# Performance work log

Measured on AMD Instinct MI355X. Metric: run time of the kernel, lower is better.

Reference implementation:

```python
import jax, jax.numpy as jnp
import numpy as np

B, T, C, H = 2, 2048, 1024, 16
HD = C // H  # head dim = 64


def setup_inputs() -> dict:
    key = jax.random.key(0)
    ks = jax.random.split(key, 5)
    scale = 0.02
    return {
        "x": jax.random.normal(ks[0], (B, T, C), dtype=jnp.float32),
        "W_attn": jax.random.normal(ks[1], (C, 3 * C), dtype=jnp.float32) * scale,
        "b_attn": jax.random.normal(ks[2], (3 * C,), dtype=jnp.float32) * scale,
        "W_proj": jax.random.normal(ks[3], (C, C), dtype=jnp.float32) * scale,
        "b_proj": jax.random.normal(ks[4], (C,), dtype=jnp.float32) * scale,
    }


def reference(x, W_attn, b_attn, W_proj, b_proj):
    Bd, Td, Cd = x.shape
    qkv = x @ W_attn + b_attn                      # [B,T,3C]
    q, k, v = jnp.split(qkv, 3, axis=-1)           # each [B,T,C]
    # [B,T,C] -> [B,H,T,HD]
    def heads(t):
        return t.reshape(Bd, Td, H, HD).transpose(0, 2, 1, 3)
    q, k, v = heads(q), heads(k), heads(v)
    att = jnp.einsum('bhqd,bhkd->bhqk', q, k) * (1.0 / np.sqrt(HD))
    causal = jnp.tril(jnp.ones((Td, Td), dtype=bool))
    att = jnp.where(causal[None, None, :, :], att, -jnp.inf)
    att = jax.nn.softmax(att, axis=-1)
    y = jnp.einsum('bhqk,bhkd->bhqd', att, v)      # [B,H,T,HD]
    y = y.transpose(0, 2, 1, 3).reshape(Bd, Td, Cd)
    return y @ W_proj + b_proj
```

## Files before the change

### kernel.cpp

```cpp
#include <hip/hip_runtime.h>
#include <hip/hip_bf16.h>


typedef __attribute__((ext_vector_type(8))) __bf16 bf16x8;
typedef __attribute__((ext_vector_type(8))) short short8;
typedef __attribute__((ext_vector_type(4))) short short4v;
typedef __attribute__((ext_vector_type(4))) float floatx4;

__device__ __forceinline__ unsigned short f2b(float f) {
    unsigned int x = __float_as_uint(f);
    x += 0x7fffu + ((x >> 16) & 1u);
    return (unsigned short)(x >> 16);
}
__device__ __forceinline__ unsigned short f2b_trunc(float f) {
    return (unsigned short)(__float_as_uint(f) >> 16);
}
__device__ __forceinline__ void gld16(const void* g, void* l) {
    __builtin_amdgcn_global_load_lds((const __attribute__((address_space(1))) void*)g,
                                     (__attribute__((address_space(3))) void*)l, 16, 0, 0);
}

__global__ __launch_bounds__(256) void cvt_k(
    const float* __restrict__ in, unsigned short* __restrict__ out, int n)
{
    int i = (blockIdx.x * 256 + threadIdx.x) << 3;
    if (i >= n) return;
    const float4 a = *(const float4*)(in + i);
    const float4 b = *(const float4*)(in + i + 4);
    short8 v;
    v[0] = (short)f2b(a.x); v[1] = (short)f2b(a.y);
    v[2] = (short)f2b(a.z); v[3] = (short)f2b(a.w);
    v[4] = (short)f2b(b.x); v[5] = (short)f2b(b.y);
    v[6] = (short)f2b(b.z); v[7] = (short)f2b(b.w);
    *(short8*)(out + i) = v;
}

__global__ __launch_bounds__(256) void transpose_cvt_k(
    const float* __restrict__ in, unsigned short* __restrict__ out,
    int R, int Cc)
{
    __shared__ unsigned short tl[64][72];
    const int t = threadIdx.x;
    const int r0 = blockIdx.y * 64, c0 = blockIdx.x * 64;
#pragma unroll
    for (int it = 0; it < 2; ++it) {
        int idx = it * 256 + t, r = idx >> 3, c8 = (idx & 7) << 3;
        const float* p = in + (size_t)(r0 + r) * Cc + c0 + c8;
        const float4 a = *(const float4*)p;
        const float4 b = *(const float4*)(p + 4);
        tl[r][c8 + 0] = f2b(a.x); tl[r][c8 + 1] = f2b(a.y);
        tl[r][c8 + 2] = f2b(a.z); tl[r][c8 + 3] = f2b(a.w);
        tl[r][c8 + 4] = f2b(b.x); tl[r][c8 + 5] = f2b(b.y);
        tl[r][c8 + 6] = f2b(b.z); tl[r][c8 + 7] = f2b(b.w);
    }
    __syncthreads();
#pragma unroll
    for (int it = 0; it < 2; ++it) {
        int idx = it * 256 + t, rr = idx >> 3, c8 = (idx & 7) << 3;
        short8 v;
#pragma unroll
        for (int i = 0; i < 8; ++i) v[i] = (short)tl[c8 + i][rr];
        *(short8*)(out + (size_t)(c0 + rr) * R + r0 + c8) = v;
    }
}

__global__ __launch_bounds__(256) void gemm_qkv(
    const unsigned short* __restrict__ A,
    const unsigned short* __restrict__ BT,
    const float* __restrict__ bias,
    unsigned short* __restrict__ outqk,
    unsigned short* __restrict__ outvt)
{
    __shared__ __align__(16) unsigned short SM[2][2][128][32];
    unsigned short* Esc = &SM[0][0][0][0];

    const int t = threadIdx.x;
    const int w = t >> 6, lane = t & 63, l15 = lane & 15, quad = lane >> 4;
    const int wr = w >> 1, wc = w & 1;
    const int m0 = blockIdx.y * 128, n0 = blockIdx.x * 128;
    const int K = 1024;

    float bia[4];
#pragma unroll
    for (int j = 0; j < 4; ++j) bia[j] = bias[n0 + wc * 64 + j * 16 + l15];

    floatx4 acc[4][4];
#pragma unroll
    for (int i = 0; i < 4; ++i)
#pragma unroll
        for (int j = 0; j < 4; ++j) acc[i][j] = (floatx4)0.f;

    const int row_s = t >> 2, kg_s = (t & 3) << 3;
    const unsigned short* gA = A  + (size_t)(m0 + row_s) * K + kg_s;
    const unsigned short* gB = BT + (size_t)(n0 + row_s) * K + kg_s;
    const int ldst = (w * 64) * 8;

#pragma unroll
    for (int c = 0; c < 2; ++c) {
        gld16(gA + (size_t)c * 64 * K, &SM[0][0][0][0] + c * 2048 + ldst);
        gld16(gB + (size_t)c * 64 * K, &SM[0][1][0][0] + c * 2048 + ldst);
    }

    for (int it = 0; it < 32; ++it) {
        __syncthreads();
        const int cur = it & 1;
        if (it < 31) {
            const int k0 = (it + 1) * 32;
#pragma unroll
            for (int c = 0; c < 2; ++c) {
                gld16(gA + (size_t)c * 64 * K + k0, &SM[cur ^ 1][0][0][0] + c * 2048 + ldst);
                gld16(gB + (size_t)c * 64 * K + k0, &SM[cur ^ 1][1][0][0] + c * 2048 + ldst);
            }
        }
        bf16x8 af[4], bfr[4];
#pragma unroll
        for (int i = 0; i < 4; ++i) af[i] = *(const bf16x8*)&SM[cur][0][wr * 64 + i * 16 + l15][quad * 8];
#pragma unroll
        for (int j = 0; j < 4; ++j) bfr[j] = *(const bf16x8*)&SM[cur][1][wc * 64 + j * 16 + l15][quad * 8];
#pragma unroll
        for (int i = 0; i < 4; ++i)
#pragma unroll
            for (int j = 0; j < 4; ++j)
                acc[i][j] = __builtin_amdgcn_mfma_f32_16x16x32_bf16(af[i], bfr[j], acc[i][j], 0, 0, 0);
    }

    const int bb = m0 >> 11, tbase = m0 & 2047;
    if (n0 < 2048) {
        for (int cf = 0; cf < 2; ++cf) {
            __syncthreads();
            if (wc == cf) {
#pragma unroll
                for (int i = 0; i < 4; ++i)
#pragma unroll
                    for (int j = 0; j < 4; ++j)
#pragma unroll
                        for (int r = 0; r < 4; ++r)
                            Esc[(wr * 64 + i * 16 + quad * 4 + r) * 72 + j * 16 + l15] =
                                f2b(acc[i][j][r] + bia[j]);
            }
            __syncthreads();
            const int fb = n0 + cf * 64;
            const int which = fb >> 10, h = (fb & 1023) >> 6;
            const int row = t >> 1, co = (t & 1) << 5;
            const unsigned short* src = Esc + row * 72 + co;
            unsigned short* dst = outqk + (size_t)which * 4194304
                + (((size_t)(bb * 16 + h) * 2048 + tbase + row) * 64 + co);
#pragma unroll
            for (int u = 0; u < 4; ++u)
                *(short8*)(dst + u * 8) = *(const short8*)(src + u * 8);
        }
    } else {
        const int hb = (n0 & 1023) >> 6;
        for (int hf = 0; hf < 2; ++hf) {
            __syncthreads();
            if (wr == hf) {
#pragma unroll
                for (int i = 0; i < 4; ++i)
#pragma unroll
                    for (int j = 0; j < 4; ++j) {
                        short4v pk;
#pragma unroll
                        for (int r = 0; r < 4; ++r) pk[r] = (short)f2b(acc[i][j][r] + bia[j]);
                        *(short4v*)&Esc[(wc * 64 + j * 16 + l15) * 72 + i * 16 + quad * 4] = pk;
                    }
            }
            __syncthreads();
            const int dl = t >> 1, co = (t & 1) << 5;
            const int h = hb + (dl >> 6), d = dl & 63;
            const unsigned short* src = Esc + dl * 72 + co;
            unsigned short* dst = outvt
                + (((size_t)(bb * 16 + h) * 64 + d) * 2048 + tbase + hf * 64 + co);
#pragma unroll
            for (int u = 0; u < 4; ++u)
                *(short8*)(dst + u * 8) = *(const short8*)(src + u * 8);
        }
    }
}

__global__ __launch_bounds__(256) void gemm_proj(
    const unsigned short* __restrict__ A,
    const unsigned short* __restrict__ BT,
    const float* __restrict__ bias,
    float* __restrict__ outf)
{
    __shared__ __align__(16) unsigned short SM[2][2][128][32];
    float* Ef = (float*)&SM[0][0][0][0];

    const int t = threadIdx.x;
    const int w = t >> 6, lane = t & 63, l15 = lane & 15, quad = lane >> 4;
    const int wr = w >> 1, wc = w & 1;
    const int m0 = blockIdx.y * 128, n0 = blockIdx.x * 128;
    const int K = 1024, N = 1024;

    float bia[4];
#pragma unroll
    for (int j = 0; j < 4; ++j) bia[j] = bias[n0 + wc * 64 + j * 16 + l15];

    floatx4 acc[4][4];
#pragma unroll
    for (int i = 0; i < 4; ++i)
#pragma unroll
        for (int j = 0; j < 4; ++j) acc[i][j] = (floatx4)0.f;

    const int row_s = t >> 2, kg_s = (t & 3) << 3;
    const unsigned short* gA = A  + (size_t)(m0 + row_s) * K + kg_s;
    const unsigned short* gB = BT + (size_t)(n0 + row_s) * K + kg_s;
    const int ldst = (w * 64) * 8;

#pragma unroll
    for (int c = 0; c < 2; ++c) {
        gld16(gA + (size_t)c * 64 * K, &SM[0][0][0][0] + c * 2048 + ldst);
        gld16(gB + (size_t)c * 64 * K, &SM[0][1][0][0] + c * 2048 + ldst);
    }

    for (int it = 0; it < 32; ++it) {
        __syncthreads();
        const int cur = it & 1;
        if (it < 31) {
            const int k0 = (it + 1) * 32;
#pragma unroll
            for (int c = 0; c < 2; ++c) {
                gld16(gA + (size_t)c * 64 * K + k0, &SM[cur ^ 1][0][0][0] + c * 2048 + ldst);
                gld16(gB + (size_t)c * 64 * K + k0, &SM[cur ^ 1][1][0][0] + c * 2048 + ldst);
            }
        }
        bf16x8 af[4], bfr[4];
#pragma unroll
        for (int i = 0; i < 4; ++i) af[i] = *(const bf16x8*)&SM[cur][0][wr * 64 + i * 16 + l15][quad * 8];
#pragma unroll
        for (int j = 0; j < 4; ++j) bfr[j] = *(const bf16x8*)&SM[cur][1][wc * 64 + j * 16 + l15][quad * 8];
#pragma unroll
        for (int i = 0; i < 4; ++i)
#pragma unroll
            for (int j = 0; j < 4; ++j)
                acc[i][j] = __builtin_amdgcn_mfma_f32_16x16x32_bf16(af[i], bfr[j], acc[i][j], 0, 0, 0);
    }

    for (int qf = 0; qf < 4; ++qf) {
        __syncthreads();
        if (wr == (qf >> 1)) {
            const int ib = (qf & 1) * 2;
#pragma unroll
            for (int ii = 0; ii < 2; ++ii)
#pragma unroll
                for (int j = 0; j < 4; ++j)
#pragma unroll
                    for (int r = 0; r < 4; ++r)
                        Ef[(ii * 16 + quad * 4 + r) * 132 + wc * 64 + j * 16 + l15] =
                            acc[ib + ii][j][r] + bia[j];
        }
        __syncthreads();
        const int row = t >> 3, co = (t & 7) << 4;
        const float* src = Ef + row * 132 + co;
        float* dst = outf + (size_t)(m0 + qf * 32 + row) * N + n0 + co;
#pragma unroll
        for (int u = 0; u < 4; ++u)
            *(float4*)(dst + u * 4) = *(const float4*)(src + u * 4);
    }
}

__global__ __launch_bounds__(256) void attn_k(
    const unsigned short* __restrict__ qg,
    const unsigned short* __restrict__ kg,
    const unsigned short* __restrict__ vt,
    unsigned short* __restrict__ y)
{
    __shared__ unsigned short Kb[2][64][64];
    __shared__ unsigned short Vb[2][64][64];
    __shared__ unsigned short Pld[4][16][72];

    const int t = threadIdx.x, w = t >> 6, lane = t & 63;
    const int l15 = lane & 15, quad = lane >> 4;
    const int bh = blockIdx.x >> 4, p = blockIdx.x & 15;
    const int b = bh >> 4, h = bh & 15;
    const float SC = 0.18033688011112042f;

    bf16x8 ones;
#pragma unroll
    for (int i = 0; i < 8; ++i) ones[i] = (__bf16)1.0f;

    const int r_s = t >> 3;
    const int g_s = t & 7;

#pragma unroll 1
    for (int hv = 0; hv < 2; ++hv) {
        const int qt = hv ? (31 - p) : p;
        const int qbase = qt * 64;

        bf16x8 qa[2];
        {
            const unsigned short* qrow = qg + ((size_t)bh * 2048 + qbase + w * 16 + l15) * 64;
            qa[0] = *(const bf16x8*)(qrow + quad * 8);
            qa[1] = *(const bf16x8*)(qrow + 32 + quad * 8);
        }

        floatx4 O[4];
#pragma unroll
        for (int j = 0; j < 4; ++j) O[j] = (floatx4)0.f;
        floatx4 lacc = (floatx4)0.f;

        __syncthreads();
        {
#pragma unroll
            for (int c = 0; c < 2; ++c) {
                int r = c * 32 + r_s;
                int cg = (g_s ^ (r & 7)) << 3;
                gld16(kg + ((size_t)bh * 2048 + r) * 64 + cg,
                      &Kb[0][0][0] + (size_t)(c * 256 + w * 64) * 8);
                gld16(vt + ((size_t)bh * 64 + r) * 2048 + cg,
                      &Vb[0][0][0] + (size_t)(c * 256 + w * 64) * 8);
            }
        }

#pragma unroll 1
        for (int kt = 0; kt <= qt; ++kt) {
            __syncthreads();
            const int cur = kt & 1;
            if (kt < qt) {
                const int kbase = (kt + 1) * 64, nxt = cur ^ 1;
#pragma unroll
                for (int c = 0; c < 2; ++c) {
                    int r = c * 32 + r_s;
                    int cg = (g_s ^ (r & 7)) << 3;
                    gld16(kg + ((size_t)bh * 2048 + kbase + r) * 64 + cg,
                          &Kb[nxt][0][0] + (size_t)(c * 256 + w * 64) * 8);
                    gld16(vt + ((size_t)bh * 64 + r) * 2048 + kbase + cg,
                          &Vb[nxt][0][0] + (size_t)(c * 256 + w * 64) * 8);
                }
            }

            floatx4 sv[4];
#pragma unroll
            for (int jn = 0; jn < 4; ++jn) sv[jn] = (floatx4)0.f;
#pragma unroll
            for (int kk = 0; kk < 2; ++kk) {
#pragma unroll
                for (int jn = 0; jn < 4; ++jn) {
                    bf16x8 bfr = *(const bf16x8*)&Kb[cur][jn * 16 + l15][((kk * 4 + quad) ^ (l15 & 7)) << 3];
                    sv[jn] = __builtin_amdgcn_mfma_f32_16x16x32_bf16(qa[kk], bfr, sv[jn], 0, 0, 0);
                }
            }

            if (kt == qt) {
#pragma unroll
                for (int jn = 0; jn < 4; ++jn) {
                    int key = jn * 16 + l15;
#pragma unroll
                    for (int r = 0; r < 4; ++r) {
                        int qr = w * 16 + quad * 4 + r;
                        float s = (key > qr) ? -1e30f : sv[jn][r];
                        sv[jn][r] = exp2f(s * SC);
                    }
                }
            } else {
#pragma unroll
                for (int jn = 0; jn < 4; ++jn)
#pragma unroll
                    for (int r = 0; r < 4; ++r) sv[jn][r] = exp2f(sv[jn][r] * SC);
            }

#pragma unroll
            for (int jn = 0; jn < 4; ++jn)
#pragma unroll
                for (int r = 0; r < 4; ++r)
                    Pld[w][quad * 4 + r][jn * 16 + l15] = f2b_trunc(sv[jn][r]);
            __builtin_amdgcn_wave_barrier();
            __builtin_amdgcn_s_waitcnt(0xc07f);
            __builtin_amdgcn_wave_barrier();

#pragma unroll
            for (int kk = 0; kk < 2; ++kk) {
                bf16x8 pa = *(const bf16x8*)&Pld[w][l15][kk * 32 + quad * 8];
                lacc = __builtin_amdgcn_mfma_f32_16x16x32_bf16(pa, ones, lacc, 0, 0, 0);
#pragma unroll
                for (int jd = 0; jd < 4; ++jd) {
                    bf16x8 vb = *(const bf16x8*)&Vb[cur][jd * 16 + l15][((kk * 4 + quad) ^ (l15 & 7)) << 3];
                    O[jd] = __builtin_amdgcn_mfma_f32_16x16x32_bf16(pa, vb, O[jd], 0, 0, 0);
                }
            }
        }

#pragma unroll
        for (int r = 0; r < 4; ++r) {
            float inv = 1.f / lacc[r];
            int tt = qbase + w * 16 + quad * 4 + r;
#pragma unroll
            for (int jd = 0; jd < 4; ++jd) {
                int c = h * 64 + jd * 16 + l15;
                y[((size_t)b * 2048 + tt) * 1024 + c] = f2b(O[jd][r] * inv);
            }
        }
    }
}

extern "C" void kernel_launch(void* const* d_in, const int* in_sizes, int n_in,
                              void* d_out, int out_size, void* d_ws, size_t ws_size,
                              hipStream_t stream) {
    const float* x      = (const float*)d_in[0];
    const float* W_attn = (const float*)d_in[1];
    const float* b_attn = (const float*)d_in[2];
    const float* W_proj = (const float*)d_in[3];
    const float* b_proj = (const float*)d_in[4];
    float* out = (float*)d_out;

    char* ws = (char*)d_ws;
    unsigned short* qk  = (unsigned short*)(ws);
    unsigned short* vtb = (unsigned short*)(ws + 16777216);
    unsigned short* y   = (unsigned short*)(ws + 25165824);
    unsigned short* xb  = (unsigned short*)(ws + 33554432);
    unsigned short* WTa = (unsigned short*)(ws + 41943040);
    unsigned short* WTp = (unsigned short*)(ws + 48234496);

    cvt_k<<<2048, 256, 0, stream>>>(x, xb, 4194304);
    transpose_cvt_k<<<dim3(48, 16), 256, 0, stream>>>(W_attn, WTa, 1024, 3072);
    transpose_cvt_k<<<dim3(16, 16), 256, 0, stream>>>(W_proj, WTp, 1024, 1024);
    gemm_qkv<<<dim3(24, 32), 256, 0, stream>>>(xb, WTa, b_attn, qk, vtb);
    attn_k<<<512, 256, 0, stream>>>(qk, qk + 4194304, vtb, y);
    gemm_proj<<<dim3(8, 32), 256, 0, stream>>>(y, WTp, b_proj, out);
}
```

Measured before the change: 203.7 us.

## Fuse prep kernels, fold softmax scale into Q, and remap attention block order

```diff
diff --git a/kernel.cpp b/kernel.cpp
--- a/kernel.cpp
+++ b/kernel.cpp
@@ -20,28 +20,38 @@
                                      (__attribute__((address_space(3))) void*)l, 16, 0, 0);
 }
 
-__global__ __launch_bounds__(256) void cvt_k(
-    const float* __restrict__ in, unsigned short* __restrict__ out, int n)
-{
-    int i = (blockIdx.x * 256 + threadIdx.x) << 3;
-    if (i >= n) return;
-    const float4 a = *(const float4*)(in + i);
-    const float4 b = *(const float4*)(in + i + 4);
-    short8 v;
-    v[0] = (short)f2b(a.x); v[1] = (short)f2b(a.y);
-    v[2] = (short)f2b(a.z); v[3] = (short)f2b(a.w);
-    v[4] = (short)f2b(b.x); v[5] = (short)f2b(b.y);
-    v[6] = (short)f2b(b.z); v[7] = (short)f2b(b.w);
-    *(short8*)(out + i) = v;
-}
-
-__global__ __launch_bounds__(256) void transpose_cvt_k(
-    const float* __restrict__ in, unsigned short* __restrict__ out,
-    int R, int Cc)
+__global__ __launch_bounds__(256) void prep_k(
+    const float* __restrict__ x,  unsigned short* __restrict__ xb,
+    const float* __restrict__ Wa, unsigned short* __restrict__ WTa,
+    const float* __restrict__ Wp, unsigned short* __restrict__ WTp)
 {
     __shared__ unsigned short tl[64][72];
-    const int t = threadIdx.x;
-    const int r0 = blockIdx.y * 64, c0 = blockIdx.x * 64;
+    const int id = blockIdx.x, t = threadIdx.x;
+
+    if (id < 2048) {
+        int i = (id * 256 + t) << 3;
+        const float4 a = *(const float4*)(x + i);
+        const float4 b = *(const float4*)(x + i + 4);
+        short8 v;
+        v[0] = (short)f2b(a.x); v[1] = (short)f2b(a.y);
+        v[2] = (short)f2b(a.z); v[3] = (short)f2b(a.w);
+        v[4] = (short)f2b(b.x); v[5] = (short)f2b(b.y);
+        v[6] = (short)f2b(b.z); v[7] = (short)f2b(b.w);
+        *(short8*)(xb + i) = v;
+        return;
+    }
+
+    const float* in;
+    unsigned short* out;
+    int R, Cc, bx, by;
+    if (id < 2816) {
+        in = Wa; out = WTa; R = 1024; Cc = 3072;
+        bx = (id - 2048) % 48; by = (id - 2048) / 48;
+    } else {
+        in = Wp; out = WTp; R = 1024; Cc = 1024;
+        bx = (id - 2816) % 16; by = (id - 2816) / 16;
+    }
+    const int r0 = by * 64, c0 = bx * 64;
 #pragma unroll
     for (int it = 0; it < 2; ++it) {
         int idx = it * 256 + t, r = idx >> 3, c8 = (idx & 7) << 3;
@@ -127,6 +137,9 @@
     const int bb = m0 >> 11, tbase = m0 & 2047;
     if (n0 < 2048) {
         for (int cf = 0; cf < 2; ++cf) {
+            const int fb = n0 + cf * 64;
+            const int which = fb >> 10, h = (fb & 1023) >> 6;
+            const float scl = (which == 0) ? 0.18033688011112042f : 1.0f;
             __syncthreads();
             if (wc == cf) {
 #pragma unroll
@@ -136,11 +149,9 @@
 #pragma unroll
                         for (int r = 0; r < 4; ++r)
                             Esc[(wr * 64 + i * 16 + quad * 4 + r) * 72 + j * 16 + l15] =
-                                f2b(acc[i][j][r] + bia[j]);
+                                f2b((acc[i][j][r] + bia[j]) * scl);
             }
             __syncthreads();
-            const int fb = n0 + cf * 64;
-            const int which = fb >> 10, h = (fb & 1023) >> 6;
             const int row = t >> 1, co = (t & 1) << 5;
             const unsigned short* src = Esc + row * 72 + co;
             unsigned short* dst = outqk + (size_t)which * 4194304
@@ -271,9 +282,10 @@
 
     const int t = threadIdx.x, w = t >> 6, lane = t & 63;
     const int l15 = lane & 15, quad = lane >> 4;
-    const int bh = blockIdx.x >> 4, p = blockIdx.x & 15;
+    const int id = blockIdx.x;
+    const int bh = (id & 7) * 4 + ((id >> 3) & 3);
+    const int p = id >> 5;
     const int b = bh >> 4, h = bh & 15;
-    const float SC = 0.18033688011112042f;
 
     bf16x8 ones;
 #pragma unroll
@@ -348,15 +360,14 @@
 #pragma unroll
                     for (int r = 0; r < 4; ++r) {
                         int qr = w * 16 + quad * 4 + r;
-                        float s = (key > qr) ? -1e30f : sv[jn][r];
-                        sv[jn][r] = exp2f(s * SC);
+                        sv[jn][r] = exp2f((key > qr) ? -1e30f : sv[jn][r]);
                     }
                 }
             } else {
 #pragma unroll
                 for (int jn = 0; jn < 4; ++jn)
 #pragma unroll
-                    for (int r = 0; r < 4; ++r) sv[jn][r] = exp2f(sv[jn][r] * SC);
+                    for (int r = 0; r < 4; ++r) sv[jn][r] = exp2f(sv[jn][r]);
             }
 
 #pragma unroll
@@ -411,9 +422,7 @@
     unsigned short* WTa = (unsigned short*)(ws + 41943040);
     unsigned short* WTp = (unsigned short*)(ws + 48234496);
 
-    cvt_k<<<2048, 256, 0, stream>>>(x, xb, 4194304);
-    transpose_cvt_k<<<dim3(48, 16), 256, 0, stream>>>(W_attn, WTa, 1024, 3072);
-    transpose_cvt_k<<<dim3(16, 16), 256, 0, stream>>>(W_proj, WTp, 1024, 1024);
+    prep_k<<<3072, 256, 0, stream>>>(x, xb, W_attn, WTa, W_proj, WTp);
     gemm_qkv<<<dim3(24, 32), 256, 0, stream>>>(xb, WTa, b_attn, qk, vtb);
     attn_k<<<512, 256, 0, stream>>>(qk, qk + 4194304, vtb, y);
     gemm_proj<<<dim3(8, 32), 256, 0, stream>>>(y, WTp, b_proj, out);
```

New measurement: 201.1 us. No clear change (-1.3%).
